# Performance work log

Hardware: AMD Instinct MI355X
Metric: run time of the kernel (lower is better)

The kernel has to match this reference:

```python
import jax, jax.numpy as jnp
import numpy as np

G = 32          # latent grid size per axis
CIN = 3         # in_channels
C = 64          # fno_hidden_channels
M = 8           # half modes per axis (n_modes=16 -> 8)
L = 4           # fno_n_layers
LIFT = 256      # fno_lifting_channels
PROJ = 256      # projection_channels
N_IN = G ** 3
N_OUT = 16384
E = 262144      # total neighbor pairs from radius search


def _gelu(x):
    return jax.nn.gelu(x, approximate=False)  # matches torch F.gelu


def _spectral_conv(x, wr, wi):
    # x: (1, Ci, G, G, G); wr/wi: (4, Ci, Co, M, M, M) -- 4 frequency corners
    xf = jnp.fft.rfftn(x, axes=(2, 3, 4), norm='forward')
    w = wr + 1j * wi
    of = jnp.zeros((x.shape[0], wr.shape[2]) + xf.shape[2:], dtype=xf.dtype)
    corners = [(slice(0, M), slice(0, M)), (slice(0, M), slice(-M, None)),
               (slice(-M, None), slice(0, M)), (slice(-M, None), slice(-M, None))]
    for k, (s1, s2) in enumerate(corners):
        of = of.at[:, :, s1, s2, :M].set(
            jnp.einsum('bixyz,ioxyz->boxyz', xf[:, :, s1, s2, :M], w[k]))
    return jnp.fft.irfftn(of, s=x.shape[2:4] + x.shape[4:], axes=(2, 3, 4), norm='forward')


def setup_inputs() -> dict:
    key = jax.random.key(0)
    ks = jax.random.split(key, 32)
    s = 0.02
    inp = {}
    inp['in_p'] = jax.random.uniform(ks[0], (G, G, G, 3), jnp.float32)
    inp['out_p'] = jax.random.uniform(ks[1], (N_OUT, 3), jnp.float32)
    inp['f'] = jax.random.normal(ks[2], (G, G, G, CIN), jnp.float32)
    inp['nb_in_idx'] = jax.random.randint(ks[3], (E,), 0, N_IN)
    inp['nb_seg'] = jnp.sort(jax.random.randint(ks[4], (E,), 0, N_OUT))
    # FNO lifting (2-layer pointwise MLP): (in+coord)=6 -> LIFT -> C
    inp['lift_w1'] = jax.random.normal(ks[5], (LIFT, CIN + 3)) * s
    inp['lift_b1'] = jnp.zeros((LIFT,), jnp.float32)
    inp['lift_w2'] = jax.random.normal(ks[6], (C, LIFT)) * s
    inp['lift_b2'] = jnp.zeros((C,), jnp.float32)
    # Spectral conv weights: (L, 4 corners, Ci, Co, M, M, M)
    sc = 1.0 / (C * C)
    inp['spec_wr'] = jax.random.normal(ks[7], (L, 4, C, C, M, M, M)) * sc
    inp['spec_wi'] = jax.random.normal(ks[8], (L, 4, C, C, M, M, M)) * sc
    inp['skip_w'] = jax.random.normal(ks[9], (L, C, C)) * s
    inp['skip_b'] = jnp.zeros((L, C), jnp.float32)
    # GNO kernel MLP: [6, 512, 256, 64]
    inp['gno_w1'] = jax.random.normal(ks[10], (512, 6)) * s
    inp['gno_b1'] = jnp.zeros((512,), jnp.float32)
    inp['gno_w2'] = jax.random.normal(ks[11], (256, 512)) * s
    inp['gno_b2'] = jnp.zeros((256,), jnp.float32)
    inp['gno_w3'] = jax.random.normal(ks[12], (C, 256)) * s
    inp['gno_b3'] = jnp.zeros((C,), jnp.float32)
    # projection MLP: C -> PROJ -> out_channels(=1)
    inp['proj_w1'] = jax.random.normal(ks[13], (PROJ, C)) * s
    inp['proj_b1'] = jnp.zeros((PROJ,), jnp.float32)
    inp['proj_w2'] = jax.random.normal(ks[14], (1, PROJ)) * s
    inp['proj_b2'] = jnp.zeros((1,), jnp.float32)
    return inp


def reference(in_p, out_p, f, nb_in_idx, nb_seg,
              lift_w1, lift_b1, lift_w2, lift_b2,
              spec_wr, spec_wi, skip_w, skip_b,
              gno_w1, gno_b1, gno_w2, gno_b2, gno_w3, gno_b3,
              proj_w1, proj_b1, proj_w2, proj_b2):
    # ---- latent_embedding: FNO over the grid ----
    x = jnp.concatenate([f, in_p], axis=-1).transpose(3, 0, 1, 2)[None]  # (1,6,G,G,G)
    x = _gelu(jnp.einsum('bixyz,oi->boxyz', x, lift_w1) + lift_b1[None, :, None, None, None])
    x = jnp.einsum('bixyz,oi->boxyz', x, lift_w2) + lift_b2[None, :, None, None, None]
    for l in range(L):
        x = (_spectral_conv(x, spec_wr[l], spec_wi[l])
             + jnp.einsum('bixyz,oi->boxyz', x, skip_w[l])
             + skip_b[l][None, :, None, None, None])
        if l < L - 1:
            x = _gelu(x)
    latent = x[0].transpose(1, 2, 3, 0).reshape(N_IN, C)  # (n_in, C)
    # ---- integrate_latent: gather -> kernel MLP -> scale by f_y -> segment mean ----
    y = in_p.reshape(N_IN, 3)
    feats = jnp.concatenate([y[nb_in_idx], out_p[nb_seg]], axis=-1)  # (E, 6)
    h = _gelu(feats @ gno_w1.T + gno_b1)
    h = _gelu(h @ gno_w2.T + gno_b2)
    kern = h @ gno_w3.T + gno_b3                     # (E, C)
    contrib = kern * latent[nb_in_idx]               # linear transform: k(x,y)*f(y)
    ssum = jax.ops.segment_sum(contrib, nb_seg, num_segments=N_OUT)
    cnt = jax.ops.segment_sum(jnp.ones((E, 1), contrib.dtype), nb_seg, num_segments=N_OUT)
    out = ssum / jnp.maximum(cnt, 1.0)               # (n_out, C)
    # ---- projection MLP ----
    h = _gelu(out @ proj_w1.T + proj_b1)
    return h @ proj_w2.T + proj_b2                   # (n_out, 1)
```

## Files before the change

### kernel.cpp

```cpp
#include <hip/hip_runtime.h>

typedef unsigned short u16;
typedef float f32x4 __attribute__((ext_vector_type(4)));
typedef _Float16 f16x8 __attribute__((ext_vector_type(8)));
typedef u16 us8 __attribute__((ext_vector_type(8)));

#define PI2f 6.283185307179586f
#define NE_TOT 262144
#define N_IN_TOT 32768
#define N_OUT_TOT 16384

__device__ __forceinline__ float gelu_f(float x){
  float t  = 0.70710678118654752f * x;
  float t2 = t * t;
  float p = t*(1.1283791670955126f + t2*(-0.37612638903183754f + t2*(0.11283791670955126f
            + t2*(-0.026866170645131253f + t2*(0.005223977625442188f + t2*(-0.0008548327023450853f))))));
  return 0.5f * x * (1.0f + p);
}
__device__ __forceinline__ float gelu_s(float x){
  float t  = 0.70710678118654752f * x;
  float t2 = t * t;
  float p = t*(1.1283791670955126f + t2*(-0.37612638903183754f + t2*(0.11283791670955126f
            + t2*(-0.026866170645131253f))));
  return 0.5f * x * (1.0f + p);
}

__device__ __forceinline__ u16 f2h(float x){
  _Float16 h = (_Float16)x;
  return __builtin_bit_cast(u16, h);
}
__device__ __forceinline__ float h2f(u16 h){
  return (float)__builtin_bit_cast(_Float16, h);
}

__global__ __launch_bounds__(256) void k_pack(const float* w2, const float* w3, u16* B2p, u16* B3p){
  int tid = blockIdx.x*256 + threadIdx.x;
  if (tid < 16*16*64*8){
    int e = tid & 7, l = (tid>>3)&63, nt = (tid>>9)&15, ks = tid>>13;
    int n = nt*16 + (l&15);
    int k = ks*32 + (l>>4)*8 + e;
    B2p[tid] = f2h(w2[n*512 + k]);
  }
  int t2 = tid - 16*16*64*8;
  if (t2 >= 0 && t2 < 8*4*64*8){
    int e = t2 & 7, l = (t2>>3)&63, nt = (t2>>9)&3, ks = t2>>11;
    int n = nt*16 + (l&15);
    int k = ks*32 + (l>>4)*8 + e;
    B3p[t2] = f2h(w3[n*256 + k]);
  }
}

__global__ __launch_bounds__(256) void k_lift(const float* f, const float* in_p,
      const float* w1, const float* b1, const float* w2, const float* b2, float* v){
  extern __shared__ char smem[];
  float* h   = (float*)smem;
  float* w2t = h + 64*256;
  float* xf  = w2t + 256*65;
  int t = threadIdx.x;
  int p0 = blockIdx.x * 64;
  for (int idx = t; idx < 64*6; idx += 256){
    int e = idx/6, k = idx - e*6;
    xf[e*8 + k] = (k < 3) ? f[(p0+e)*3 + k] : in_p[(p0+e)*3 + (k-3)];
  }
  for (int i4 = t; i4 < 4096; i4 += 256){
    const float4 wv = ((const float4*)w2)[i4];
    int c = i4 >> 6, u = (i4 & 63)*4;
    w2t[(u+0)*65 + c] = wv.x;
    w2t[(u+1)*65 + c] = wv.y;
    w2t[(u+2)*65 + c] = wv.z;
    w2t[(u+3)*65 + c] = wv.w;
  }
  __syncthreads();
  {
    int u = t;
    float wr[6];
    #pragma unroll
    for (int k = 0; k < 6; ++k) wr[k] = w1[u*6 + k];
    float bb = b1[u];
    for (int e = 0; e < 64; ++e){
      float s = bb;
      #pragma unroll
      for (int k = 0; k < 6; ++k) s += wr[k]*xf[e*8+k];
      h[e*256 + u] = gelu_f(s);
    }
  }
  __syncthreads();
  {
    int c = t & 63, zg = t >> 6;
    float acc[16];
    #pragma unroll
    for (int i=0;i<16;++i) acc[i]=0.f;
    for (int u4 = 0; u4 < 64; ++u4){
      float wv0 = w2t[(u4*4+0)*65 + c];
      float wv1 = w2t[(u4*4+1)*65 + c];
      float wv2 = w2t[(u4*4+2)*65 + c];
      float wv3 = w2t[(u4*4+3)*65 + c];
      #pragma unroll
      for (int ee = 0; ee < 16; ++ee){
        const float4 hv = *(const float4*)&h[(zg*16+ee)*256 + u4*4];
        acc[ee] += wv0*hv.x + wv1*hv.y + wv2*hv.z + wv3*hv.w;
      }
    }
    float bb = b2[c];
    #pragma unroll
    for (int ee = 0; ee < 16; ++ee)
      v[(size_t)(p0 + zg*16 + ee)*64 + c] = acc[ee] + bb;
  }
}

__global__ __launch_bounds__(256) void k_s1(const float* v, float* T1){
  __shared__ float vt[2048];
  __shared__ float twc[256], tws[256];
  int t = threadIdx.x;
  int xy = blockIdx.x;
  {
    int kz = t >> 5, z = t & 31;
    float sv, cv;
    sincosf(PI2f * (float)(kz*z) / 32.0f, &sv, &cv);
    twc[t] = cv; tws[t] = sv;
  }
  for (int i4 = t; i4 < 512; i4 += 256)
    ((float4*)vt)[i4] = ((const float4*)(v + (size_t)xy*2048))[i4];
  __syncthreads();
  int c = t & 63, kzg = t >> 6;
  int kza = kzg, kzb = kzg + 4;
  float re0=0,im0=0,re1=0,im1=0;
  for (int z = 0; z < 32; ++z){
    float vv = vt[z*64 + c];
    re0 += vv * twc[kza*32+z]; im0 -= vv * tws[kza*32+z];
    re1 += vv * twc[kzb*32+z]; im1 -= vv * tws[kzb*32+z];
  }
  const float sc = 1.0f/32768.0f;
  float2* o = (float2*)T1;
  o[(xy*8 + kza)*64 + c] = make_float2(re0*sc, im0*sc);
  o[(xy*8 + kzb)*64 + c] = make_float2(re1*sc, im1*sc);
}

__global__ __launch_bounds__(256) void k_s2(const float* T1, float* T2){
  __shared__ float t1s[2048];
  __shared__ float twc[512], tws[512];
  int t = threadIdx.x;
  int x = blockIdx.x >> 4, kz = (blockIdx.x >> 1) & 7, ch = blockIdx.x & 1;
  for (int i = t; i < 512; i += 256){
    int kyi = i >> 5, y = i & 31;
    int ky = (kyi < 8) ? kyi : kyi + 16;
    float sv, cv; sincosf(PI2f * (float)(ky*y) / 32.0f, &sv, &cv);
    twc[i]=cv; tws[i]=sv;
  }
  for (int i4 = t; i4 < 512; i4 += 256){
    int y = i4 >> 4, q4 = i4 & 15;
    ((float4*)t1s)[i4] = *((const float4*)&T1[((size_t)((x*32+y)*8 + kz))*128 + ch*64] + q4);
  }
  __syncthreads();
  int cl = t & 31, g = t >> 5;
  float ar[2], ai[2];
  ar[0]=0;ar[1]=0;ai[0]=0;ai[1]=0;
  for (int y = 0; y < 32; ++y){
    float tr = t1s[(y*32+cl)*2], ti = t1s[(y*32+cl)*2+1];
    #pragma unroll
    for (int kk = 0; kk < 2; ++kk){
      int kyi = g + kk*8;
      float cc = twc[kyi*32+y], ss = tws[kyi*32+y];
      ar[kk] += tr*cc + ti*ss;
      ai[kk] += ti*cc - tr*ss;
    }
  }
  float2* o = (float2*)T2;
  int c = ch*32 + cl;
  #pragma unroll
  for (int kk = 0; kk < 2; ++kk){
    int kyi = g + kk*8;
    o[((x*16 + kyi)*8 + kz)*64 + c] = make_float2(ar[kk], ai[kk]);
  }
}

__global__ __launch_bounds__(256) void k_s3(const float* T2, float* F){
  __shared__ float t2s[1024];
  __shared__ float twc[512], tws[512];
  int t = threadIdx.x;
  int kyi = blockIdx.x >> 5, kz = (blockIdx.x >> 2) & 7, cq = blockIdx.x & 3;
  for (int i = t; i < 512; i += 256){
    int kxi = i >> 5, x = i & 31;
    int kx = (kxi < 8) ? kxi : kxi + 16;
    float sv, cv; sincosf(PI2f * (float)(kx*x) / 32.0f, &sv, &cv);
    twc[i]=cv; tws[i]=sv;
  }
  if (t < 256){
    int i4 = t;
    int x = i4 >> 3, q4 = i4 & 7;
    ((float4*)t2s)[i4] = *((const float4*)&T2[((size_t)((x*16+kyi)*8 + kz))*128 + cq*32] + q4);
  }
  __syncthreads();
  int cl = t & 15, kxi = t >> 4;
  float ar = 0.f, ai = 0.f;
  for (int x = 0; x < 32; ++x){
    float tr = t2s[(x*16+cl)*2], ti = t2s[(x*16+cl)*2+1];
    float cc = twc[kxi*32+x], ss = tws[kxi*32+x];
    ar += tr*cc + ti*ss;
    ai += ti*cc - tr*ss;
  }
  float2* o = (float2*)F;
  int c = cq*16 + cl;
  o[((kxi*16 + kyi)*8 + kz)*64 + c] = make_float2(ar, ai);
}

__global__ __launch_bounds__(256) void k_s4(const float* F, const float* wr, const float* wi, float* OFp){
  __shared__ float FT[16*65*2];
  int t = threadIdx.x;
  int bid = blockIdx.x;
  int oh = bid & 7, ic = (bid>>3)&3, mx = (bid>>6)&7, corner = bid>>9;
  int kxi = (corner>>1)*8 + mx;
  int kyb = (corner&1)*8;
  for (int idx = t; idx < 2048; idx += 256){
    int m = idx >> 5, w = idx & 31;
    int cl = w >> 1, part = w & 1;
    int my = m >> 3, kz = m & 7;
    FT[(cl*65 + m)*2 + part] = F[((size_t)((kxi*16 + kyb + my)*8 + kz))*128 + ic*32 + w];
  }
  __syncthreads();
  int m = t & 63, og = t >> 6;
  int my = m >> 3, kz = m & 7;
  float accr[2], acci[2];
  accr[0]=0;accr[1]=0;acci[0]=0;acci[1]=0;
  #pragma unroll 4
  for (int i = 0; i < 16; ++i){
    float fr = FT[(i*65+m)*2], fi = FT[(i*65+m)*2+1];
    size_t rowbase = ((size_t)(corner*64 + ic*16 + i))*64;
    #pragma unroll
    for (int oo = 0; oo < 2; ++oo){
      int o = oh*8 + og*2 + oo;
      size_t widx = (rowbase + o)*512 + mx*64 + m;
      float wrv = wr[widx], wiv = wi[widx];
      accr[oo] += wrv*fr - wiv*fi;
      acci[oo] += wrv*fi + wiv*fr;
    }
  }
  float2* o2 = (float2*)OFp;
  size_t obase = (size_t)ic*131072 + ((size_t)((kxi*16 + kyb + my)*8 + kz))*64;
  #pragma unroll
  for (int oo = 0; oo < 2; ++oo){
    int o = oh*8 + og*2 + oo;
    o2[obase + o] = make_float2(accr[oo], acci[oo]);
  }
}

__global__ __launch_bounds__(256) void k_s5(const float* OFp, float* G1){
  __shared__ float OFs[512];
  __shared__ float twc[512], tws[512];
  int t = threadIdx.x;
  int kyi = blockIdx.x >> 5, kz = (blockIdx.x >> 2) & 7, oq = blockIdx.x & 3;
  for (int i = t; i < 512; i += 256){
    int kxi = i >> 5, x = i & 31;
    int kx = (kxi < 8) ? kxi : kxi + 16;
    float sv, cv; sincosf(PI2f * (float)(kx*x) / 32.0f, &sv, &cv);
    twc[i]=cv; tws[i]=sv;
  }
  if (t < 128){
    int i4 = t;
    int kx = i4 >> 3, w4 = i4 & 7;
    float4 s = {0.f,0.f,0.f,0.f};
    #pragma unroll
    for (int p = 0; p < 4; ++p){
      const float4 vv = *((const float4*)&OFp[(size_t)p*262144 + ((size_t)((kx*16+kyi)*8+kz))*128 + oq*32] + w4);
      s.x += vv.x; s.y += vv.y; s.z += vv.z; s.w += vv.w;
    }
    ((float4*)OFs)[i4] = s;
  }
  __syncthreads();
  int ol = t & 15, g = t >> 4;
  float ar[2], ai[2];
  ar[0]=0;ar[1]=0;ai[0]=0;ai[1]=0;
  for (int kxi = 0; kxi < 16; ++kxi){
    float orr = OFs[(kxi*16+ol)*2], oii = OFs[(kxi*16+ol)*2+1];
    #pragma unroll
    for (int xx = 0; xx < 2; ++xx){
      int x = g + xx*16;
      float cc = twc[kxi*32+x], ss = tws[kxi*32+x];
      ar[xx] += orr*cc - oii*ss;
      ai[xx] += orr*ss + oii*cc;
    }
  }
  float2* o2 = (float2*)G1;
  int o = oq*16 + ol;
  #pragma unroll
  for (int xx = 0; xx < 2; ++xx){
    int x = g + xx*16;
    o2[((x*16 + kyi)*8 + kz)*64 + o] = make_float2(ar[xx], ai[xx]);
  }
}

__global__ __launch_bounds__(256) void k_s6(const float* G1, float* G2){
  __shared__ float g1s[1024];
  __shared__ float twc[512], tws[512];
  int t = threadIdx.x;
  int x = blockIdx.x >> 4, kz = (blockIdx.x >> 1) & 7, oh = blockIdx.x & 1;
  for (int i = t; i < 512; i += 256){
    int kyi = i >> 5, y = i & 31;
    int ky = (kyi < 8) ? kyi : kyi + 16;
    float sv, cv; sincosf(PI2f * (float)(ky*y) / 32.0f, &sv, &cv);
    twc[i]=cv; tws[i]=sv;
  }
  if (t < 256){
    int i4 = t;
    int kyi = i4 >> 4, w4 = i4 & 15;
    ((float4*)g1s)[i4] = *((const float4*)&G1[((size_t)((x*16+kyi)*8+kz))*128 + oh*64] + w4);
  }
  __syncthreads();
  int ol = t & 31, g = t >> 5;
  float ar[4], ai[4];
  #pragma unroll
  for (int i=0;i<4;++i){ar[i]=0;ai[i]=0;}
  for (int kyi = 0; kyi < 16; ++kyi){
    float gr = g1s[(kyi*32+ol)*2], gi = g1s[(kyi*32+ol)*2+1];
    #pragma unroll
    for (int yy = 0; yy < 4; ++yy){
      int y = g + yy*8;
      float cc = twc[kyi*32+y], ss = tws[kyi*32+y];
      ar[yy] += gr*cc - gi*ss;
      ai[yy] += gr*ss + gi*cc;
    }
  }
  float2* o2 = (float2*)G2;
  int o = oh*32 + ol;
  #pragma unroll
  for (int yy = 0; yy < 4; ++yy){
    int y = g + yy*8;
    o2[((x*32 + y)*8 + kz)*64 + o] = make_float2(ar[yy], ai[yy]);
  }
}

__global__ __launch_bounds__(256) void k_s7(const float* G2, const float* vin,
      const float* skw, const float* skb, float* vout, int dogelu){
  __shared__ float g2s[1024];
  __shared__ float vt[2048];
  __shared__ float wT[64*65];
  __shared__ float twc[256], tws[256];
  __shared__ float sb[64];
  int t = threadIdx.x;
  int xy = blockIdx.x;
  {
    int kz = t >> 5, z = t & 31;
    float sv, cv; sincosf(PI2f * (float)(kz*z) / 32.0f, &sv, &cv);
    twc[t]=cv; tws[t]=sv;
  }
  { int i4 = t; if (i4 < 256) ((float4*)g2s)[i4] = ((const float4*)(G2 + (size_t)xy*1024))[i4]; }
  for (int i4 = t; i4 < 512; i4 += 256)
    ((float4*)vt)[i4] = ((const float4*)(vin + (size_t)xy*2048))[i4];
  for (int i4 = t; i4 < 1024; i4 += 256){
    const float4 wv = ((const float4*)skw)[i4];
    int cc = i4 >> 4, ii = (i4 & 15)*4;
    wT[(ii+0)*65 + cc] = wv.x;
    wT[(ii+1)*65 + cc] = wv.y;
    wT[(ii+2)*65 + cc] = wv.z;
    wT[(ii+3)*65 + cc] = wv.w;
  }
  if (t < 64) sb[t] = skb[t];
  __syncthreads();
  int c = t & 63, zg = t >> 6;
  float accz[8];
  #pragma unroll
  for (int zz=0; zz<8; ++zz){
    int z = zg*8 + zz;
    float s = g2s[c*2];
    #pragma unroll
    for (int kz=1; kz<8; ++kz){
      float gr = g2s[(kz*64+c)*2], gi = g2s[(kz*64+c)*2+1];
      s += 2.0f*(gr*twc[kz*32+z] - gi*tws[kz*32+z]);
    }
    accz[zz] = s + sb[c];
  }
  for (int i4 = 0; i4 < 16; ++i4){
    float w0 = wT[(i4*4+0)*65 + c];
    float w1v = wT[(i4*4+1)*65 + c];
    float w2v = wT[(i4*4+2)*65 + c];
    float w3v = wT[(i4*4+3)*65 + c];
    #pragma unroll
    for (int zz=0; zz<8; ++zz){
      const float4 vv = *(const float4*)&vt[(zg*8+zz)*64 + i4*4];
      accz[zz] += w0*vv.x + w1v*vv.y + w2v*vv.z + w3v*vv.w;
    }
  }
  #pragma unroll
  for (int zz=0; zz<8; ++zz){
    float s = accz[zz];
    if (dogelu) s = gelu_f(s);
    vout[(size_t)(xy*32 + zg*8 + zz)*64 + c] = s;
  }
}

__global__ __launch_bounds__(256, 4) void k_gno(
    const int* nb_i, const int* nb_j, const float* in_p, const float* out_p,
    const float* w1, const float* b1, const float* b2g, const float* b3g,
    const u16* B2p, const u16* B3p, const float* latent, float* ssum){
  extern __shared__ char smem[];
  u16*   h1c   = (u16*)smem;
  u16*   h2s   = (u16*)smem;
  float* feats = (float*)(smem + 32768);
  float* sb2   = feats + 512;
  float* sb3   = sb2 + 256;
  int*   idxE  = (int*)(sb3 + 64);
  int*   segE  = idxE + 64;
  int t = threadIdx.x;
  int e0 = blockIdx.x * 64;
  if (t < 64){
    int gi = nb_i[e0 + t];
    int gj = nb_j[e0 + t];
    idxE[t] = gi;
    segE[t] = gj;
    feats[t*8+0] = in_p[gi*3+0];
    feats[t*8+1] = in_p[gi*3+1];
    feats[t*8+2] = in_p[gi*3+2];
    feats[t*8+3] = out_p[gj*3+0];
    feats[t*8+4] = out_p[gj*3+1];
    feats[t*8+5] = out_p[gj*3+2];
    sb3[t] = b3g[t];
  }
  sb2[t] = b2g[t];
  int l = t & 63, w = t >> 6;
  int up = t & 63;
  int eg = t >> 6;
  f32x4 acc[4][4];
  #pragma unroll
  for (int m=0;m<4;++m)
    #pragma unroll
    for (int n=0;n<4;++n) acc[m][n] = (f32x4){0.f,0.f,0.f,0.f};
  __syncthreads();

  for (int chunk = 0; chunk < 4; ++chunk){
    int u0 = chunk*128 + up*2;
    float wa[6], wb[6];
    #pragma unroll
    for (int k=0;k<6;++k){ wa[k]=w1[u0*6+k]; wb[k]=w1[u0*6+6+k]; }
    float ba = b1[u0], bb = b1[u0+1];
    #pragma unroll 4
    for (int n = 0; n < 16; ++n){
      int e = eg*16 + n;
      const float4 fa = *(const float4*)&feats[e*8];
      const float4 fb = *(const float4*)&feats[e*8+4];
      float s0 = ba + wa[0]*fa.x + wa[1]*fa.y + wa[2]*fa.z + wa[3]*fa.w + wa[4]*fb.x + wa[5]*fb.y;
      float s1 = bb + wb[0]*fa.x + wb[1]*fa.y + wb[2]*fa.z + wb[3]*fa.w + wb[4]*fb.x + wb[5]*fb.y;
      unsigned lo = f2h(gelu_s(s0));
      unsigned hi = f2h(gelu_s(s1));
      int bofs = (e*256 + up*4) ^ ((e&7)<<4);
      *(unsigned*)((char*)h1c + bofs) = lo | (hi<<16);
    }
    __syncthreads();
    #pragma unroll
    for (int ks2 = 0; ks2 < 4; ++ks2){
      int gk = chunk*4 + ks2;
      f16x8 af[4];
      #pragma unroll
      for (int m=0;m<4;++m){
        int row = m*16 + (l&15);
        int bofs = (row*256 + ks2*64 + (l>>4)*16) ^ ((row&7)<<4);
        af[m] = __builtin_bit_cast(f16x8, *(const us8*)((const char*)h1c + bofs));
      }
      f16x8 bq[4];
      #pragma unroll
      for (int nt=0;nt<4;++nt){
        int ntg = w*4 + nt;
        bq[nt] = __builtin_bit_cast(f16x8, *(const us8*)(B2p + ((gk*16 + ntg)*64 + l)*8));
      }
      #pragma unroll
      for (int m=0;m<4;++m)
        #pragma unroll
        for (int nt=0;nt<4;++nt)
          acc[m][nt] = __builtin_amdgcn_mfma_f32_16x16x32_f16(af[m], bq[nt], acc[m][nt], 0, 0, 0);
    }
    __syncthreads();
  }

  #pragma unroll
  for (int m=0;m<4;++m){
    #pragma unroll
    for (int nt=0;nt<4;++nt){
      #pragma unroll
      for (int r=0;r<4;++r){
        int row = m*16 + (l>>4)*4 + r;
        int n = w*64 + nt*16 + (l&15);
        float vv = gelu_s(acc[m][nt][r] + sb2[n]);
        int bofs = (row*512 + n*2) ^ ((row&7)<<4);
        *(u16*)((char*)h2s + bofs) = f2h(vv);
      }
    }
  }
  __syncthreads();
  f32x4 a3[4];
  #pragma unroll
  for (int m=0;m<4;++m) a3[m] = (f32x4){0.f,0.f,0.f,0.f};
  #pragma unroll
  for (int ks = 0; ks < 8; ++ks){
    f16x8 bq3 = __builtin_bit_cast(f16x8, *(const us8*)(B3p + ((ks*4 + w)*64 + l)*8));
    #pragma unroll
    for (int m=0;m<4;++m){
      int row = m*16 + (l&15);
      int bofs = (row*512 + ks*64 + (l>>4)*16) ^ ((row&7)<<4);
      f16x8 am = __builtin_bit_cast(f16x8, *(const us8*)((const char*)h2s + bofs));
      a3[m] = __builtin_amdgcn_mfma_f32_16x16x32_f16(am, bq3, a3[m], 0, 0, 0);
    }
  }
  {
    int q = l >> 4;
    int c = w*16 + (l&15);
    float b3c = sb3[c];
    float pend = 0.f;
    int pseg = -1;
    #pragma unroll
    for (int m=0;m<4;++m){
      #pragma unroll
      for (int r=0;r<4;++r){
        int e = m*16 + q*4 + r;
        float kern = a3[m][r] + b3c;
        float val = kern * latent[(size_t)idxE[e]*64 + c];
        int sg = segE[e];
        if (sg != pseg){
          if (pseg >= 0) atomicAdd(&ssum[(size_t)pseg*64 + c], pend);
          pseg = sg; pend = val;
        } else {
          pend += val;
        }
      }
    }
    atomicAdd(&ssum[(size_t)pseg*64 + c], pend);
  }
}

__global__ __launch_bounds__(256) void k_proj(const int* seg, const float* ssum,
                                              const float* w1, const float* b1,
                                              const float* w2, const float* b2, float* out){
  __shared__ float rows[64*68];
  __shared__ float w1s[256*68];
  __shared__ float w2s[256];
  __shared__ float b1s[256];
  __shared__ float red[256];
  __shared__ float invE[64];
  int t = threadIdx.x;
  int r0 = blockIdx.x * 64;
  if (t < 64){
    int j = r0 + t;
    int lo = 0, hi = NE_TOT;
    while (lo < hi){ int mid = (lo+hi)>>1; if (seg[mid] < j) lo = mid+1; else hi = mid; }
    int s0 = lo;
    hi = NE_TOT;
    while (lo < hi){ int mid = (lo+hi)>>1; if (seg[mid] < j+1) lo = mid+1; else hi = mid; }
    invE[t] = 1.0f / fmaxf((float)(lo - s0), 1.0f);
  }
  __syncthreads();
  for (int idx = t; idx < 4096; idx += 256){
    int e = idx >> 6, c = idx & 63;
    rows[e*68 + c] = ssum[(size_t)(r0+e)*64 + c] * invE[e];
  }
  for (int idx = t; idx < 16384; idx += 256){
    int u = idx >> 6, c = idx & 63;
    w1s[u*68 + c] = w1[idx];
  }
  w2s[t] = w2[t];
  b1s[t] = b1[t];
  __syncthreads();
  int e = t >> 2, q = t & 3;
  float fsum = 0.f;
  for (int uu = 0; uu < 64; ++uu){
    int u = uu*4 + q;
    float pre = b1s[u];
    #pragma unroll
    for (int c4 = 0; c4 < 16; ++c4){
      const float4 a = *(const float4*)&w1s[u*68 + c4*4];
      const float4 r = *(const float4*)&rows[e*68 + c4*4];
      pre += a.x*r.x + a.y*r.y + a.z*r.z + a.w*r.w;
    }
    fsum += w2s[u] * gelu_f(pre);
  }
  red[t] = fsum;
  __syncthreads();
  if (t < 64){
    out[r0 + t] = red[t*4] + red[t*4+1] + red[t*4+2] + red[t*4+3] + b2[0];
  }
}

extern "C" void kernel_launch(void* const* d_in, const int* in_sizes, int n_in,
                              void* d_out, int out_size, void* d_ws, size_t ws_size,
                              hipStream_t stream){
  const float* in_p  = (const float*)d_in[0];
  const float* out_p = (const float*)d_in[1];
  const float* f     = (const float*)d_in[2];
  const int*   nb_i  = (const int*)d_in[3];
  const int*   nb_j  = (const int*)d_in[4];
  const float* lw1   = (const float*)d_in[5];
  const float* lb1   = (const float*)d_in[6];
  const float* lw2   = (const float*)d_in[7];
  const float* lb2   = (const float*)d_in[8];
  const float* swr   = (const float*)d_in[9];
  const float* swi   = (const float*)d_in[10];
  const float* skw   = (const float*)d_in[11];
  const float* skb   = (const float*)d_in[12];
  const float* gw1   = (const float*)d_in[13];
  const float* gb1   = (const float*)d_in[14];
  const float* gw2   = (const float*)d_in[15];
  const float* gb2   = (const float*)d_in[16];
  const float* gw3   = (const float*)d_in[17];
  const float* gb3   = (const float*)d_in[18];
  const float* pw1   = (const float*)d_in[19];
  const float* pb1   = (const float*)d_in[20];
  const float* pw2   = (const float*)d_in[21];
  const float* pb2   = (const float*)d_in[22];
  float* out = (float*)d_out;

  char* ws = (char*)d_ws;
  size_t off = 0;
  auto alloc = [&](size_t bytes)->void*{ void* p = ws + off; off += (bytes + 255) & ~(size_t)255; return p; };
  float* va      = (float*)alloc((size_t)N_IN_TOT*64*4);
  float* vb      = (float*)alloc((size_t)N_IN_TOT*64*4);
  float* T1      = (float*)alloc((size_t)32*32*8*64*2*4);
  float* T2      = (float*)alloc((size_t)32*16*8*64*2*4);
  float* Fq      = (float*)alloc((size_t)16*16*8*64*2*4);
  float* OFp     = (float*)alloc((size_t)4*16*16*8*64*2*4);
  float* G1      = (float*)alloc((size_t)32*16*8*64*2*4);
  float* G2      = (float*)alloc((size_t)32*32*8*64*2*4);
  u16*   B2p     = (u16*)alloc((size_t)16*16*64*8*2);
  u16*   B3p     = (u16*)alloc((size_t)8*4*64*8*2);
  float* ssum    = (float*)alloc((size_t)N_OUT_TOT*64*4);

  hipMemsetAsync(d_ws, 0, off, stream);

  k_pack<<<576, 256, 0, stream>>>(gw2, gw3, B2p, B3p);
  k_lift<<<512, 256, 134144, stream>>>(f, in_p, lw1, lb1, lw2, lb2, va);

  float* vin = va; float* vout = vb;
  for (int layer = 0; layer < 4; ++layer){
    k_s1<<<1024, 256, 0, stream>>>(vin, T1);
    k_s2<<<512, 256, 0, stream>>>(T1, T2);
    k_s3<<<512, 256, 0, stream>>>(T2, Fq);
    k_s4<<<1024, 256, 0, stream>>>(Fq, swr + (size_t)layer*4*64*64*512, swi + (size_t)layer*4*64*64*512, OFp);
    k_s5<<<512, 256, 0, stream>>>(OFp, G1);
    k_s6<<<512, 256, 0, stream>>>(G1, G2);
    k_s7<<<1024, 256, 0, stream>>>(G2, vin, skw + layer*64*64, skb + layer*64, vout, (layer < 3) ? 1 : 0);
    float* tmp = vin; vin = vout; vout = tmp;
  }
  k_gno<<<4096, 256, 36608, stream>>>(nb_i, nb_j, in_p, out_p, gw1, gb1, gb2, gb3,
                                      B2p, B3p, vin, ssum);
  k_proj<<<256, 256, 0, stream>>>(nb_j, ssum, pw1, pb1, pw2, pb2, out);
}
```

Baseline: 559.3 us.

## Fuse first z-DFT stage into lift/skip kernels and replace atomic segment sum

The first spectral stage (z-axis DFT) is folded into the lifting kernel and into the skip/GELU epilogue of layers 0-2, which removes a separate launch and a re-read of the activation volume per layer. The GNO kernel now writes per-edge contributions to a 64 MB buffer instead of doing run-length atomic adds into the segment sums. A new segment-mean kernel reduces those contributions by binary-searching segment bounds, and the workspace memset is dropped. This avoids atomics and zero-initialisation but adds a large extra write and read of edge contributions.

```diff
diff --git a/kernel.cpp b/kernel.cpp
--- a/kernel.cpp
+++ b/kernel.cpp
@@ -50,12 +50,15 @@
   }
 }
 
-__global__ __launch_bounds__(256) void k_lift(const float* f, const float* in_p,
-      const float* w1, const float* b1, const float* w2, const float* b2, float* v){
+__global__ __launch_bounds__(256) void k_lift_s1(const float* f, const float* in_p,
+      const float* w1, const float* b1, const float* w2, const float* b2, float* v, float* T1){
   extern __shared__ char smem[];
   float* h   = (float*)smem;
   float* w2t = h + 64*256;
   float* xf  = w2t + 256*65;
+  float* vt2 = h;
+  float* twc = xf;
+  float* tws = xf + 256;
   int t = threadIdx.x;
   int p0 = blockIdx.x * 64;
   for (int idx = t; idx < 64*6; idx += 256){
@@ -86,8 +89,14 @@
   }
   __syncthreads();
   {
-    int c = t & 63, zg = t >> 6;
-    float acc[16];
+    int kz = t >> 5, z = t & 31;
+    float sv, cv;
+    sincosf(PI2f * (float)(kz*z) / 32.0f, &sv, &cv);
+    twc[t] = cv; tws[t] = sv;
+  }
+  int c = t & 63, zg = t >> 6;
+  float acc[16];
+  {
     #pragma unroll
     for (int i=0;i<16;++i) acc[i]=0.f;
     for (int u4 = 0; u4 < 64; ++u4){
@@ -101,39 +110,36 @@
         acc[ee] += wv0*hv.x + wv1*hv.y + wv2*hv.z + wv3*hv.w;
       }
     }
+  }
+  __syncthreads();
+  {
     float bb = b2[c];
     #pragma unroll
-    for (int ee = 0; ee < 16; ++ee)
-      v[(size_t)(p0 + zg*16 + ee)*64 + c] = acc[ee] + bb;
-  }
-}
-
-__global__ __launch_bounds__(256) void k_s1(const float* v, float* T1){
-  __shared__ float vt[2048];
-  __shared__ float twc[256], tws[256];
-  int t = threadIdx.x;
-  int xy = blockIdx.x;
-  {
-    int kz = t >> 5, z = t & 31;
-    float sv, cv;
-    sincosf(PI2f * (float)(kz*z) / 32.0f, &sv, &cv);
-    twc[t] = cv; tws[t] = sv;
-  }
-  for (int i4 = t; i4 < 512; i4 += 256)
-    ((float4*)vt)[i4] = ((const float4*)(v + (size_t)xy*2048))[i4];
-  __syncthreads();
-  int c = t & 63, kzg = t >> 6;
+    for (int ee = 0; ee < 16; ++ee){
+      float val = acc[ee] + bb;
+      int pl = zg*16 + ee;
+      v[(size_t)(p0 + pl)*64 + c] = val;
+      vt2[pl*64 + c] = val;
+    }
+  }
+  __syncthreads();
+  const float sc = 1.0f/32768.0f;
+  int kzg = t >> 6;
   int kza = kzg, kzb = kzg + 4;
-  float re0=0,im0=0,re1=0,im1=0;
-  for (int z = 0; z < 32; ++z){
-    float vv = vt[z*64 + c];
-    re0 += vv * twc[kza*32+z]; im0 -= vv * tws[kza*32+z];
-    re1 += vv * twc[kzb*32+z]; im1 -= vv * tws[kzb*32+z];
-  }
-  const float sc = 1.0f/32768.0f;
   float2* o = (float2*)T1;
-  o[(xy*8 + kza)*64 + c] = make_float2(re0*sc, im0*sc);
-  o[(xy*8 + kzb)*64 + c] = make_float2(re1*sc, im1*sc);
+  #pragma unroll
+  for (int xyl = 0; xyl < 2; ++xyl){
+    const float* vt = vt2 + xyl*2048;
+    int xy = blockIdx.x*2 + xyl;
+    float re0=0,im0=0,re1=0,im1=0;
+    for (int z = 0; z < 32; ++z){
+      float vv = vt[z*64 + c];
+      re0 += vv * twc[kza*32+z]; im0 -= vv * tws[kza*32+z];
+      re1 += vv * twc[kzb*32+z]; im1 -= vv * tws[kzb*32+z];
+    }
+    o[(xy*8 + kza)*64 + c] = make_float2(re0*sc, im0*sc);
+    o[(xy*8 + kzb)*64 + c] = make_float2(re1*sc, im1*sc);
+  }
 }
 
 __global__ __launch_bounds__(256) void k_s2(const float* T1, float* T2){
@@ -329,8 +335,8 @@
   }
 }
 
-__global__ __launch_bounds__(256) void k_s7(const float* G2, const float* vin,
-      const float* skw, const float* skb, float* vout, int dogelu){
+__global__ __launch_bounds__(256) void k_s7s1(const float* G2, const float* vin,
+      const float* skw, const float* skb, float* vout, float* T1){
   __shared__ float g2s[1024];
   __shared__ float vt[2048];
   __shared__ float wT[64*65];
@@ -380,6 +386,82 @@
       accz[zz] += w0*vv.x + w1v*vv.y + w2v*vv.z + w3v*vv.w;
     }
   }
+  __syncthreads();
+  #pragma unroll
+  for (int zz=0; zz<8; ++zz){
+    float s = gelu_f(accz[zz]);
+    int z = zg*8 + zz;
+    vout[(size_t)(xy*32 + z)*64 + c] = s;
+    vt[z*64 + c] = s;
+  }
+  __syncthreads();
+  {
+    const float sc = 1.0f/32768.0f;
+    int kzg = t >> 6;
+    int kza = kzg, kzb = kzg + 4;
+    float re0=0,im0=0,re1=0,im1=0;
+    for (int z = 0; z < 32; ++z){
+      float vv = vt[z*64 + c];
+      re0 += vv * twc[kza*32+z]; im0 -= vv * tws[kza*32+z];
+      re1 += vv * twc[kzb*32+z]; im1 -= vv * tws[kzb*32+z];
+    }
+    float2* o = (float2*)T1;
+    o[(xy*8 + kza)*64 + c] = make_float2(re0*sc, im0*sc);
+    o[(xy*8 + kzb)*64 + c] = make_float2(re1*sc, im1*sc);
+  }
+}
+
+__global__ __launch_bounds__(256) void k_s7(const float* G2, const float* vin,
+      const float* skw, const float* skb, float* vout, int dogelu){
+  __shared__ float g2s[1024];
+  __shared__ float vt[2048];
+  __shared__ float wT[64*65];
+  __shared__ float twc[256], tws[256];
+  __shared__ float sb[64];
+  int t = threadIdx.x;
+  int xy = blockIdx.x;
+  {
+    int kz = t >> 5, z = t & 31;
+    float sv, cv; sincosf(PI2f * (float)(kz*z) / 32.0f, &sv, &cv);
+    twc[t]=cv; tws[t]=sv;
+  }
+  { int i4 = t; if (i4 < 256) ((float4*)g2s)[i4] = ((const float4*)(G2 + (size_t)xy*1024))[i4]; }
+  for (int i4 = t; i4 < 512; i4 += 256)
+    ((float4*)vt)[i4] = ((const float4*)(vin + (size_t)xy*2048))[i4];
+  for (int i4 = t; i4 < 1024; i4 += 256){
+    const float4 wv = ((const float4*)skw)[i4];
+    int cc = i4 >> 4, ii = (i4 & 15)*4;
+    wT[(ii+0)*65 + cc] = wv.x;
+    wT[(ii+1)*65 + cc] = wv.y;
+    wT[(ii+2)*65 + cc] = wv.z;
+    wT[(ii+3)*65 + cc] = wv.w;
+  }
+  if (t < 64) sb[t] = skb[t];
+  __syncthreads();
+  int c = t & 63, zg = t >> 6;
+  float accz[8];
+  #pragma unroll
+  for (int zz=0; zz<8; ++zz){
+    int z = zg*8 + zz;
+    float s = g2s[c*2];
+    #pragma unroll
+    for (int kz=1; kz<8; ++kz){
+      float gr = g2s[(kz*64+c)*2], gi = g2s[(kz*64+c)*2+1];
+      s += 2.0f*(gr*twc[kz*32+z] - gi*tws[kz*32+z]);
+    }
+    accz[zz] = s + sb[c];
+  }
+  for (int i4 = 0; i4 < 16; ++i4){
+    float w0 = wT[(i4*4+0)*65 + c];
+    float w1v = wT[(i4*4+1)*65 + c];
+    float w2v = wT[(i4*4+2)*65 + c];
+    float w3v = wT[(i4*4+3)*65 + c];
+    #pragma unroll
+    for (int zz=0; zz<8; ++zz){
+      const float4 vv = *(const float4*)&vt[(zg*8+zz)*64 + i4*4];
+      accz[zz] += w0*vv.x + w1v*vv.y + w2v*vv.z + w3v*vv.w;
+    }
+  }
   #pragma unroll
   for (int zz=0; zz<8; ++zz){
     float s = accz[zz];
@@ -391,7 +473,7 @@
 __global__ __launch_bounds__(256, 4) void k_gno(
     const int* nb_i, const int* nb_j, const float* in_p, const float* out_p,
     const float* w1, const float* b1, const float* b2g, const float* b3g,
-    const u16* B2p, const u16* B3p, const float* latent, float* ssum){
+    const u16* B2p, const u16* B3p, const float* latent, float* contrib){
   extern __shared__ char smem[];
   u16*   h1c   = (u16*)smem;
   u16*   h2s   = (u16*)smem;
@@ -399,14 +481,12 @@
   float* sb2   = feats + 512;
   float* sb3   = sb2 + 256;
   int*   idxE  = (int*)(sb3 + 64);
-  int*   segE  = idxE + 64;
   int t = threadIdx.x;
   int e0 = blockIdx.x * 64;
   if (t < 64){
     int gi = nb_i[e0 + t];
     int gj = nb_j[e0 + t];
     idxE[t] = gi;
-    segE[t] = gj;
     feats[t*8+0] = in_p[gi*3+0];
     feats[t*8+1] = in_p[gi*3+1];
     feats[t*8+2] = in_p[gi*3+2];
@@ -503,52 +583,45 @@
     int q = l >> 4;
     int c = w*16 + (l&15);
     float b3c = sb3[c];
-    float pend = 0.f;
-    int pseg = -1;
     #pragma unroll
     for (int m=0;m<4;++m){
       #pragma unroll
       for (int r=0;r<4;++r){
         int e = m*16 + q*4 + r;
         float kern = a3[m][r] + b3c;
-        float val = kern * latent[(size_t)idxE[e]*64 + c];
-        int sg = segE[e];
-        if (sg != pseg){
-          if (pseg >= 0) atomicAdd(&ssum[(size_t)pseg*64 + c], pend);
-          pseg = sg; pend = val;
-        } else {
-          pend += val;
-        }
+        contrib[((size_t)(e0+e))*64 + c] = kern * latent[(size_t)idxE[e]*64 + c];
       }
     }
-    atomicAdd(&ssum[(size_t)pseg*64 + c], pend);
-  }
-}
-
-__global__ __launch_bounds__(256) void k_proj(const int* seg, const float* ssum,
-                                              const float* w1, const float* b1,
+  }
+}
+
+__global__ __launch_bounds__(256) void k_segmean(const int* seg, const float* contrib, float* outseg){
+  int t = threadIdx.x;
+  int j = blockIdx.x*4 + (t>>6);
+  int lane = t & 63;
+  int lo = 0, hi = NE_TOT;
+  while (lo < hi){ int mid = (lo+hi)>>1; if (seg[mid] < j) lo = mid+1; else hi = mid; }
+  int s0 = lo;
+  hi = NE_TOT;
+  while (lo < hi){ int mid = (lo+hi)>>1; if (seg[mid] < j+1) lo = mid+1; else hi = mid; }
+  int s1 = lo;
+  float s = 0.f;
+  for (int e = s0; e < s1; ++e) s += contrib[(size_t)e*64 + lane];
+  outseg[(size_t)j*64 + lane] = s / fmaxf((float)(s1 - s0), 1.0f);
+}
+
+__global__ __launch_bounds__(256) void k_proj(const float* outseg, const float* w1, const float* b1,
                                               const float* w2, const float* b2, float* out){
   __shared__ float rows[64*68];
   __shared__ float w1s[256*68];
   __shared__ float w2s[256];
   __shared__ float b1s[256];
   __shared__ float red[256];
-  __shared__ float invE[64];
   int t = threadIdx.x;
   int r0 = blockIdx.x * 64;
-  if (t < 64){
-    int j = r0 + t;
-    int lo = 0, hi = NE_TOT;
-    while (lo < hi){ int mid = (lo+hi)>>1; if (seg[mid] < j) lo = mid+1; else hi = mid; }
-    int s0 = lo;
-    hi = NE_TOT;
-    while (lo < hi){ int mid = (lo+hi)>>1; if (seg[mid] < j+1) lo = mid+1; else hi = mid; }
-    invE[t] = 1.0f / fmaxf((float)(lo - s0), 1.0f);
-  }
-  __syncthreads();
   for (int idx = t; idx < 4096; idx += 256){
     int e = idx >> 6, c = idx & 63;
-    rows[e*68 + c] = ssum[(size_t)(r0+e)*64 + c] * invE[e];
+    rows[e*68 + c] = outseg[(size_t)(r0+e)*64 + c];
   }
   for (int idx = t; idx < 16384; idx += 256){
     int u = idx >> 6, c = idx & 63;
@@ -618,25 +691,28 @@
   float* G2      = (float*)alloc((size_t)32*32*8*64*2*4);
   u16*   B2p     = (u16*)alloc((size_t)16*16*64*8*2);
   u16*   B3p     = (u16*)alloc((size_t)8*4*64*8*2);
-  float* ssum    = (float*)alloc((size_t)N_OUT_TOT*64*4);
-
-  hipMemsetAsync(d_ws, 0, off, stream);
+  float* contrib = (float*)alloc((size_t)NE_TOT*64*4);
+  float* outseg  = (float*)alloc((size_t)N_OUT_TOT*64*4);
+
 
   k_pack<<<576, 256, 0, stream>>>(gw2, gw3, B2p, B3p);
-  k_lift<<<512, 256, 134144, stream>>>(f, in_p, lw1, lb1, lw2, lb2, va);
+  k_lift_s1<<<512, 256, 134144, stream>>>(f, in_p, lw1, lb1, lw2, lb2, va, T1);
 
   float* vin = va; float* vout = vb;
   for (int layer = 0; layer < 4; ++layer){
-    k_s1<<<1024, 256, 0, stream>>>(vin, T1);
     k_s2<<<512, 256, 0, stream>>>(T1, T2);
     k_s3<<<512, 256, 0, stream>>>(T2, Fq);
     k_s4<<<1024, 256, 0, stream>>>(Fq, swr + (size_t)layer*4*64*64*512, swi + (size_t)layer*4*64*64*512, OFp);
     k_s5<<<512, 256, 0, stream>>>(OFp, G1);
     k_s6<<<512, 256, 0, stream>>>(G1, G2);
-    k_s7<<<1024, 256, 0, stream>>>(G2, vin, skw + layer*64*64, skb + layer*64, vout, (layer < 3) ? 1 : 0);
+    if (layer < 3)
+      k_s7s1<<<1024, 256, 0, stream>>>(G2, vin, skw + layer*64*64, skb + layer*64, vout, T1);
+    else
+      k_s7<<<1024, 256, 0, stream>>>(G2, vin, skw + layer*64*64, skb + layer*64, vout, 0);
     float* tmp = vin; vin = vout; vout = tmp;
   }
   k_gno<<<4096, 256, 36608, stream>>>(nb_i, nb_j, in_p, out_p, gw1, gb1, gb2, gb3,
-                                      B2p, B3p, vin, ssum);
-  k_proj<<<256, 256, 0, stream>>>(nb_j, ssum, pw1, pb1, pw2, pb2, out);
-}
+                                      B2p, B3p, vin, contrib);
+  k_segmean<<<4096, 256, 0, stream>>>(nb_j, contrib, outseg);
+  k_proj<<<256, 256, 0, stream>>>(outseg, pw1, pb1, pw2, pb2, out);
+}
```

Result: faster. 478.6 us, median of 2 (-14.4%).
